# Optimization experiments

Measured on AMD Instinct MI355X. Metric: run time of the kernel, lower is better.

Reference implementation:

```python
import jax, jax.numpy as jnp
import numpy as np

HID = 256
NUM_ENT = 100000
NUM_REL = 50
E = 320000  # edges per direction; edge_index has 2*E columns
BN_EPS = 1e-5


def setup_inputs() -> dict:
    key = jax.random.key(0)
    ks = jax.random.split(key, 10)
    x = jax.random.normal(ks[0], (NUM_ENT, HID), dtype=jnp.float32)
    edge_index = jax.random.randint(ks[1], (2, 2 * E), 0, NUM_ENT)
    edge_type = jax.random.randint(ks[2], (2 * E,), 0, NUM_REL)
    rel_embed = jax.random.normal(ks[3], (NUM_REL, HID), dtype=jnp.float32)
    # xavier_normal init: std = sqrt(2 / (fan_in + fan_out))
    w_std = (2.0 / (HID + HID)) ** 0.5
    w_loop = jax.random.normal(ks[4], (HID, HID), dtype=jnp.float32) * w_std
    w_in = jax.random.normal(ks[5], (HID, HID), dtype=jnp.float32) * w_std
    w_out = jax.random.normal(ks[6], (HID, HID), dtype=jnp.float32) * w_std
    w_rel = jax.random.normal(ks[7], (HID, HID), dtype=jnp.float32) * w_std
    loop_rel = jax.random.normal(ks[8], (1, HID), dtype=jnp.float32) * ((2.0 / (1 + HID)) ** 0.5)
    bn_weight = jnp.ones((HID,), dtype=jnp.float32)
    bn_bias = jnp.zeros((HID,), dtype=jnp.float32)
    return {
        "x": x, "edge_index": edge_index, "edge_type": edge_type,
        "rel_embed": rel_embed, "w_loop": w_loop, "w_in": w_in,
        "w_out": w_out, "w_rel": w_rel, "loop_rel": loop_rel,
        "bn_weight": bn_weight, "bn_bias": bn_bias,
    }


def _compute_norm(edge_index, num_ent):
    # symmetric D^-1/2 * D^-1/2 norm; degree counted on row (target) index
    row, col = edge_index[0], edge_index[1]
    deg = jax.ops.segment_sum(jnp.ones_like(row, dtype=jnp.float32), row, num_segments=num_ent)
    deg_inv = jnp.where(deg > 0, deg ** -0.5, 0.0)
    return deg_inv[row] * deg_inv[col]


def _propagate(x, idx, etype, rel_all, W, norm, num_ent):
    # gather source nodes (idx[1]), compose with relation emb (mult), transform, scale, scatter-add to targets (idx[0])
    msg = (x[idx[1]] * rel_all[etype]) @ W  # [E, d]
    if norm is not None:
        msg = msg * norm[:, None]
    return jax.ops.segment_sum(msg, idx[0], num_segments=num_ent)


def reference(x, edge_index, edge_type, rel_embed, w_loop, w_in, w_out, w_rel,
              loop_rel, bn_weight, bn_bias):
    num_ent = x.shape[0]
    rel_all = jnp.concatenate([rel_embed, loop_rel], axis=0)  # [R+1, d]
    e = edge_index.shape[1] // 2
    in_index, out_index = edge_index[:, :e], edge_index[:, e:]
    in_type, out_type = edge_type[:e], edge_type[e:]

    in_norm = _compute_norm(in_index, num_ent)
    out_norm = _compute_norm(out_index, num_ent)

    in_res = _propagate(x, in_index, in_type, rel_all, w_in, in_norm, num_ent)
    out_res = _propagate(x, out_index, out_type, rel_all, w_out, out_norm, num_ent)
    # self-loop: identity scatter -> just per-node compose+transform
    loop_res = (x * loop_rel) @ w_loop

    out = (in_res + out_res + loop_res) * (1.0 / 3.0)

    # BatchNorm1d in training mode (batch stats, biased variance)
    mean = out.mean(axis=0)
    var = out.var(axis=0)
    out = (out - mean) * jax.lax.rsqrt(var + BN_EPS) * bn_weight + bn_bias

    rel_out = (rel_all @ w_rel)[:-1]  # drop loop relation
    return out, rel_out
```

## Files before the change

kernel.cpp:

```cpp
#include <hip/hip_runtime.h>

#define HID     256
#define N_ENT   100000
#define TOT_E   640000
#define HALF_E  320000
#define NSEG    (2 * N_ENT)
#define BN_EPSF 1e-5f
#define SCAN_ELEMS 1024
#define NBLK_SCAN  ((NSEG + SCAN_ELEMS - 1) / SCAN_ELEMS)

typedef short bf16x8 __attribute__((ext_vector_type(8)));
typedef short bf16x4 __attribute__((ext_vector_type(4)));
typedef float f32x4  __attribute__((ext_vector_type(4)));

__device__ __forceinline__ short f2b(float f) {
    union { float f; unsigned u; } c; c.f = f;
    unsigned u = c.u;
    u += 0x7FFF + ((u >> 16) & 1);
    return (short)(u >> 16);
}
__device__ __forceinline__ float b2f(short b) {
    union { unsigned u; float f; } c;
    c.u = ((unsigned)(unsigned short)b) << 16;
    return c.f;
}

#define NX8 (N_ENT * HID / 8)
#define NR8 (50 * HID / 8)
#define CONV_BLOCKS ((NX8 + NR8 + 255) / 256)
__global__ void prep_kernel(const float* __restrict__ x, short* __restrict__ xh,
                            const float* __restrict__ rel, short* __restrict__ relh,
                            const float* __restrict__ w_in, const float* __restrict__ w_out,
                            const float* __restrict__ w_loop, const float* __restrict__ loop_rel,
                            short* __restrict__ WT,
                            int* __restrict__ offs, float* __restrict__ stats) {
    int bid = blockIdx.x;
    int tid = threadIdx.x;
    if (bid < CONV_BLOCKS) {
        int i = bid * 256 + tid;
        if (i < NSEG) offs[i] = 0;
        if (i < 512) stats[i] = 0.f;
        const float* src; short* dst; int idx;
        if (i < NX8) { src = x; dst = xh; idx = i; }
        else if (i < NX8 + NR8) { src = rel; dst = relh; idx = i - NX8; }
        else return;
        const float4* p = (const float4*)(src + (size_t)idx * 8);
        float4 v0 = p[0], v1 = p[1];
        bf16x8 pk;
        pk[0]=f2b(v0.x); pk[1]=f2b(v0.y); pk[2]=f2b(v0.z); pk[3]=f2b(v0.w);
        pk[4]=f2b(v1.x); pk[5]=f2b(v1.y); pk[6]=f2b(v1.z); pk[7]=f2b(v1.w);
        *(bf16x8*)(dst + (size_t)idx * 8) = pk;
    } else {
        int n = bid - CONV_BLOCKS;
        int t = tid;
        float v0 = w_in  [(size_t)t * HID + n];
        float v1 = w_out [(size_t)t * HID + n];
        float v2 = w_loop[(size_t)t * HID + n] * loop_rel[t];
        short* row = WT + (size_t)n * 768;
        row[t]       = f2b(v0);
        row[256 + t] = f2b(v1);
        row[512 + t] = f2b(v2);
    }
}

__global__ void hist_kernel(const int* __restrict__ ei, int* __restrict__ offs) {
    int j = blockIdx.x * 256 + threadIdx.x;
    if (j >= TOT_E) return;
    int seg = ei[j] + ((j < HALF_E) ? 0 : N_ENT);
    atomicAdd(&offs[seg], 1);
}

__global__ __launch_bounds__(256) void scan1(int* __restrict__ offs, int* __restrict__ bsums,
                                             float* __restrict__ rnorm) {
    __shared__ int tsum[256];
    int b = blockIdx.x, t = threadIdx.x;
    int base = b * SCAN_ELEMS + t * 4;
    int v[4] = {0, 0, 0, 0};
    if (base + 3 < NSEG) {
        int4 lv = *(const int4*)(offs + base);
        v[0] = lv.x; v[1] = lv.y; v[2] = lv.z; v[3] = lv.w;
    } else {
        for (int i = 0; i < 4; ++i) if (base + i < NSEG) v[i] = offs[base + i];
    }
    #pragma unroll
    for (int i = 0; i < 4; ++i)
        if (base + i < NSEG)
            rnorm[base + i] = (v[i] > 0) ? rsqrtf((float)v[i]) : 0.f;
    tsum[t] = v[0] + v[1] + v[2] + v[3];
    __syncthreads();
    for (int d = 1; d < 256; d <<= 1) {
        int val = (t >= d) ? tsum[t - d] : 0;
        __syncthreads();
        tsum[t] += val;
        __syncthreads();
    }
    int run = (t == 0) ? 0 : tsum[t - 1];
    if (t == 255) bsums[b] = tsum[255];
    int w[4];
    for (int i = 0; i < 4; ++i) { w[i] = run; run += v[i]; }
    if (base + 3 < NSEG) *(int4*)(offs + base) = make_int4(w[0], w[1], w[2], w[3]);
    else for (int i = 0; i < 4; ++i) if (base + i < NSEG) offs[base + i] = w[i];
}

__global__ __launch_bounds__(256) void scan3f(int* __restrict__ offs, const int* __restrict__ bsums) {
    __shared__ int tmp[256];
    int b = blockIdx.x, t = threadIdx.x;
    tmp[t] = (t < NBLK_SCAN) ? bsums[t] : 0;
    __syncthreads();
    for (int d = 1; d < 256; d <<= 1) {
        int val = (t >= d) ? tmp[t - d] : 0;
        __syncthreads();
        tmp[t] += val;
        __syncthreads();
    }
    int add = (b == 0) ? 0 : tmp[b - 1];
    int base = b * SCAN_ELEMS + t * 4;
    if (base + 3 < NSEG) {
        int4 v = *(int4*)(offs + base);
        v.x += add; v.y += add; v.z += add; v.w += add;
        *(int4*)(offs + base) = v;
    } else {
        for (int i = 0; i < 4; ++i) if (base + i < NSEG) offs[base + i] += add;
    }
}

__global__ void fill8_kernel(const int* __restrict__ ei, const int* __restrict__ et,
                             int* __restrict__ offs, const float* __restrict__ rnorm,
                             int2* __restrict__ elist8) {
    int j = blockIdx.x * 256 + threadIdx.x;
    if (j >= TOT_E) return;
    int hb  = (j < HALF_E) ? 0 : N_ENT;
    int seg = ei[j] + hb;
    int col = ei[TOT_E + j];
    float norm = rnorm[seg] * rnorm[hb + col];
    int pos = atomicAdd(&offs[seg], 1);
    elist8[pos] = make_int2(col | (et[j] << 17), __float_as_int(norm));
}

__global__ __launch_bounds__(256) void gather_h(
        const short* __restrict__ xh, const short* __restrict__ relh,
        const int* __restrict__ offs, const int2* __restrict__ elist8,
        short* __restrict__ accA, short* __restrict__ accB) {
    int s = blockIdx.x * 4 + (threadIdx.x >> 6);
    int lane = threadIdx.x & 63;
    int start = (s == 0) ? 0 : offs[s - 1];
    int end   = offs[s];
    float ax0=0.f, ay0=0.f, az0=0.f, aw0=0.f;
    float ax1=0.f, ay1=0.f, az1=0.f, aw1=0.f;
    int e = start;
    for (; e + 2 <= end; e += 2) {
        int2 p0 = elist8[e];
        int2 p1 = elist8[e + 1];
        int   c0 = p0.x & 0x1FFFF, t0 = p0.x >> 17;
        float n0 = __int_as_float(p0.y);
        int   c1 = p1.x & 0x1FFFF, t1 = p1.x >> 17;
        float n1 = __int_as_float(p1.y);
        bf16x4 xv0 = *(const bf16x4*)(xh   + (size_t)c0 * HID + lane * 4);
        bf16x4 rv0 = *(const bf16x4*)(relh + (size_t)t0 * HID + lane * 4);
        bf16x4 xv1 = *(const bf16x4*)(xh   + (size_t)c1 * HID + lane * 4);
        bf16x4 rv1 = *(const bf16x4*)(relh + (size_t)t1 * HID + lane * 4);
        ax0 += b2f(xv0[0]) * b2f(rv0[0]) * n0;
        ay0 += b2f(xv0[1]) * b2f(rv0[1]) * n0;
        az0 += b2f(xv0[2]) * b2f(rv0[2]) * n0;
        aw0 += b2f(xv0[3]) * b2f(rv0[3]) * n0;
        ax1 += b2f(xv1[0]) * b2f(rv1[0]) * n1;
        ay1 += b2f(xv1[1]) * b2f(rv1[1]) * n1;
        az1 += b2f(xv1[2]) * b2f(rv1[2]) * n1;
        aw1 += b2f(xv1[3]) * b2f(rv1[3]) * n1;
    }
    if (e < end) {
        int2 p = elist8[e];
        int   c = p.x & 0x1FFFF, t = p.x >> 17;
        float n = __int_as_float(p.y);
        bf16x4 xv = *(const bf16x4*)(xh   + (size_t)c * HID + lane * 4);
        bf16x4 rv = *(const bf16x4*)(relh + (size_t)t * HID + lane * 4);
        ax0 += b2f(xv[0]) * b2f(rv[0]) * n;
        ay0 += b2f(xv[1]) * b2f(rv[1]) * n;
        az0 += b2f(xv[2]) * b2f(rv[2]) * n;
        aw0 += b2f(xv[3]) * b2f(rv[3]) * n;
    }
    int hb = (s >= N_ENT) ? N_ENT : 0;
    short* dst = ((s >= N_ENT) ? accB : accA) + (size_t)(s - hb) * HID + lane * 4;
    bf16x4 pk;
    pk[0] = f2b(ax0 + ax1); pk[1] = f2b(ay0 + ay1);
    pk[2] = f2b(az0 + az1); pk[3] = f2b(aw0 + aw1);
    *(bf16x4*)dst = pk;
}

template <bool BF16OUT>
__global__ __launch_bounds__(256) void gemm_mfma_h(
        const short* __restrict__ accA, const short* __restrict__ accB,
        const short* __restrict__ xh, const short* __restrict__ WT,
        float* __restrict__ out, short* __restrict__ outh, float* __restrict__ stats)
{
    __shared__ __align__(16) short As[64 * 64];
    __shared__ __align__(16) short Bs[256 * 64];
    const int tid = threadIdx.x;
    const int l   = tid & 63;
    const int wid = tid >> 6;
    const int r0  = blockIdx.x * 64;
    const int lr  = l & 15;
    const int lg  = l >> 4;

    f32x4 acc[4][4];
    #pragma unroll
    for (int i = 0; i < 4; ++i)
        #pragma unroll
        for (int j = 0; j < 4; ++j)
            acc[i][j] = (f32x4){0.f, 0.f, 0.f, 0.f};

    const int sg = tid & 7;
    const int sr = tid >> 3;

    for (int kt = 0; kt < 12; ++kt) {
        const int src = kt >> 2;
        const short* Ap = (src == 0) ? accA : ((src == 1) ? accB : xh);
        const int ksg = kt * 64;
        const int ksl = (kt & 3) * 64;
        __syncthreads();
        #pragma unroll
        for (int h = 0; h < 2; ++h) {
            int r  = sr + 32 * h;
            int gr = r0 + r;
            bf16x8 v = {0,0,0,0,0,0,0,0};
            if (gr < N_ENT) v = *(const bf16x8*)(Ap + (size_t)gr * HID + ksl + sg * 8);
            *(bf16x8*)&As[r * 64 + ((sg ^ (r & 7)) << 3)] = v;
        }
        #pragma unroll
        for (int i = 0; i < 8; ++i) {
            int n = sr + 32 * i;
            bf16x8 w = *(const bf16x8*)(WT + (size_t)n * 768 + ksg + sg * 8);
            *(bf16x8*)&Bs[n * 64 + ((sg ^ (n & 7)) << 3)] = w;
        }
        __syncthreads();
        #pragma unroll
        for (int kc = 0; kc < 2; ++kc) {
            const int gsel = kc * 4 + lg;
            bf16x8 af[4], bfr[4];
            #pragma unroll
            for (int i = 0; i < 4; ++i) {
                int r = 16 * i + lr;
                af[i] = *(const bf16x8*)&As[r * 64 + ((gsel ^ (r & 7)) << 3)];
            }
            #pragma unroll
            for (int j = 0; j < 4; ++j) {
                int n = wid * 64 + 16 * j + lr;
                bfr[j] = *(const bf16x8*)&Bs[n * 64 + ((gsel ^ (n & 7)) << 3)];
            }
            #pragma unroll
            for (int i = 0; i < 4; ++i)
                #pragma unroll
                for (int j = 0; j < 4; ++j)
                    acc[i][j] = __builtin_amdgcn_mfma_f32_16x16x32_bf16(
                                    af[i], bfr[j], acc[i][j], 0, 0, 0);
        }
    }

    const float third = 1.f / 3.f;
    float s[4]  = {0.f, 0.f, 0.f, 0.f};
    float sq[4] = {0.f, 0.f, 0.f, 0.f};
    #pragma unroll
    for (int i = 0; i < 4; ++i) {
        #pragma unroll
        for (int v = 0; v < 4; ++v) {
            int grow = r0 + 16 * i + lg * 4 + v;
            if (grow < N_ENT) {
                #pragma unroll
                for (int j = 0; j < 4; ++j) {
                    float val = acc[i][j][v] * third;
                    int col = wid * 64 + 16 * j + lr;
                    if (BF16OUT) outh[(size_t)grow * HID + col] = f2b(val);
                    else         out [(size_t)grow * HID + col] = val;
                    s[j] += val; sq[j] += val * val;
                }
            }
        }
    }
    #pragma unroll
    for (int j = 0; j < 4; ++j) {
        s[j]  += __shfl_xor(s[j], 16);  s[j]  += __shfl_xor(s[j], 32);
        sq[j] += __shfl_xor(sq[j], 16); sq[j] += __shfl_xor(sq[j], 32);
    }
    if (lg == 0) {
        #pragma unroll
        for (int j = 0; j < 4; ++j) {
            int c = wid * 64 + 16 * j + lr;
            atomicAdd(&stats[c], s[j]);
            atomicAdd(&stats[HID + c], sq[j]);
        }
    }
}

#define BN_BLOCKS 1024
__global__ void bn_relout_h(const short* __restrict__ outh, float* __restrict__ out,
                            const float* __restrict__ stats,
                            const float* __restrict__ bnw, const float* __restrict__ bnb,
                            const float* __restrict__ rel_embed, const float* __restrict__ w_rel,
                            float* __restrict__ rel_out) {
    if (blockIdx.x < BN_BLOCKS) {
        const float invN = 1.f / (float)N_ENT;
        const int total8 = N_ENT * (HID / 8);
        for (int i = blockIdx.x * 256 + threadIdx.x; i < total8; i += BN_BLOCKS * 256) {
            int c = (i & 31) * 8;
            bf16x8 v = *(const bf16x8*)(outh + (size_t)i * 8);
            float r[8];
            #pragma unroll
            for (int k = 0; k < 8; ++k) {
                float mean = stats[c + k] * invN;
                float var  = stats[HID + c + k] * invN - mean * mean;
                float sc   = rsqrtf(var + BN_EPSF) * bnw[c + k];
                float sh   = bnb[c + k] - mean * sc;
                r[k] = b2f(v[k]) * sc + sh;
            }
            float4* dst = (float4*)(out + (size_t)i * 8);
            dst[0] = make_float4(r[0], r[1], r[2], r[3]);
            dst[1] = make_float4(r[4], r[5], r[6], r[7]);
        }
    } else {
        __shared__ float row[HID];
        int r = blockIdx.x - BN_BLOCKS;
        int c = threadIdx.x;
        row[c] = rel_embed[(size_t)r * HID + c];
        __syncthreads();
        float sum = 0.f;
        #pragma unroll 8
        for (int k = 0; k < HID; ++k) sum += row[k] * w_rel[(size_t)k * HID + c];
        rel_out[(size_t)r * HID + c] = sum;
    }
}

__global__ void bn_relout_f(float* __restrict__ out, const float* __restrict__ stats,
                            const float* __restrict__ bnw, const float* __restrict__ bnb,
                            const float* __restrict__ rel_embed, const float* __restrict__ w_rel,
                            float* __restrict__ rel_out) {
    if (blockIdx.x < BN_BLOCKS) {
        const float invN = 1.f / (float)N_ENT;
        const int total4 = N_ENT * (HID / 4);
        for (int i = blockIdx.x * 256 + threadIdx.x; i < total4; i += BN_BLOCKS * 256) {
            int c = (i & 63) * 4;
            float4 v = *(float4*)(out + (size_t)i * 4);
            #pragma unroll
            for (int k = 0; k < 4; ++k) {
                float mean = stats[c + k] * invN;
                float var  = stats[HID + c + k] * invN - mean * mean;
                float sc   = rsqrtf(var + BN_EPSF) * bnw[c + k];
                float sh   = bnb[c + k] - mean * sc;
                float* comp = (k == 0) ? &v.x : (k == 1) ? &v.y : (k == 2) ? &v.z : &v.w;
                *comp = (*comp) * sc + sh;
            }
            *(float4*)(out + (size_t)i * 4) = v;
        }
    } else {
        __shared__ float row[HID];
        int r = blockIdx.x - BN_BLOCKS;
        int c = threadIdx.x;
        row[c] = rel_embed[(size_t)r * HID + c];
        __syncthreads();
        float sum = 0.f;
        #pragma unroll 8
        for (int k = 0; k < HID; ++k) sum += row[k] * w_rel[(size_t)k * HID + c];
        rel_out[(size_t)r * HID + c] = sum;
    }
}

extern "C" void kernel_launch(void* const* d_in, const int* in_sizes, int n_in,
                              void* d_out, int out_size, void* d_ws, size_t ws_size,
                              hipStream_t stream) {
    const float* x        = (const float*)d_in[0];
    const int*   ei       = (const int*)d_in[1];
    const int*   et       = (const int*)d_in[2];
    const float* rel      = (const float*)d_in[3];
    const float* w_loop   = (const float*)d_in[4];
    const float* w_in     = (const float*)d_in[5];
    const float* w_out    = (const float*)d_in[6];
    const float* w_rel    = (const float*)d_in[7];
    const float* loop_rel = (const float*)d_in[8];
    const float* bnw      = (const float*)d_in[9];
    const float* bnb      = (const float*)d_in[10];

    float* out     = (float*)d_out;
    float* rel_out = out + (size_t)N_ENT * HID;

    const size_t XH_B   = (size_t)N_ENT * HID * 2;
    const size_t ACC_B  = (size_t)N_ENT * HID * 2;
    const size_t OFFS_B = (size_t)NSEG * 4;
    const size_t EL8_B  = (size_t)TOT_E * 8;
    const size_t RN_B   = (size_t)NSEG * 4;
    const size_t RELH_B = (size_t)50 * HID * 2;
    const size_t WT_B   = (size_t)256 * 768 * 2;
    const size_t base_need = XH_B + 2 * ACC_B + OFFS_B + EL8_B + RN_B
                           + 256 * 4 + 512 * 4 + RELH_B + WT_B;
    const size_t OUTH_B = (size_t)N_ENT * HID * 2;
    const bool   have_outh = (ws_size >= base_need + OUTH_B);

    char* w = (char*)d_ws;
    short* xh     = (short*)w;              w += XH_B;
    short* accA_h = (short*)w;              w += ACC_B;
    short* accB_h = (short*)w;              w += ACC_B;
    int*   offs   = (int*)w;                w += OFFS_B;
    int2*  elist8 = (int2*)w;               w += EL8_B;
    float* rnorm  = (float*)w;              w += RN_B;
    int*   bsums  = (int*)w;                w += 256 * 4;
    float* stats  = (float*)w;              w += 512 * 4;
    short* relh   = (short*)w;              w += RELH_B;
    short* WT     = (short*)w;              w += WT_B;
    short* outh   = (short*)w;

    prep_kernel<<<CONV_BLOCKS + 256, 256, 0, stream>>>(x, xh, rel, relh,
                                                       w_in, w_out, w_loop, loop_rel,
                                                       WT, offs, stats);
    hist_kernel<<<TOT_E / 256, 256, 0, stream>>>(ei, offs);
    scan1<<<NBLK_SCAN, 256, 0, stream>>>(offs, bsums, rnorm);
    scan3f<<<NBLK_SCAN, 256, 0, stream>>>(offs, bsums);
    fill8_kernel<<<TOT_E / 256, 256, 0, stream>>>(ei, et, offs, rnorm, elist8);
    gather_h<<<NSEG / 4, 256, 0, stream>>>(xh, relh, offs, elist8, accA_h, accB_h);
    if (have_outh) {
        gemm_mfma_h<true><<<(N_ENT + 63) / 64, 256, 0, stream>>>(
            accA_h, accB_h, xh, WT, out, outh, stats);
        bn_relout_h<<<BN_BLOCKS + 50, 256, 0, stream>>>(outh, out, stats, bnw, bnb,
                                                        rel, w_rel, rel_out);
    } else {
        gemm_mfma_h<false><<<(N_ENT + 63) / 64, 256, 0, stream>>>(
            accA_h, accB_h, xh, WT, out, outh, stats);
        bn_relout_f<<<BN_BLOCKS + 50, 256, 0, stream>>>(out, stats, bnw, bnb,
                                                        rel, w_rel, rel_out);
    }
}
```

Before: 308.4 us.

## Triple-buffer GEMM tiles with direct global-to-LDS async loads

```diff
diff --git a/kernel.cpp b/kernel.cpp
--- a/kernel.cpp
+++ b/kernel.cpp
@@ -23,6 +23,11 @@
     union { unsigned u; float f; } c;
     c.u = ((unsigned)(unsigned short)b) << 16;
     return c.f;
+}
+__device__ __forceinline__ void gload16(const void* g, void* l) {
+    __builtin_amdgcn_global_load_lds(
+        (const __attribute__((address_space(1))) unsigned*)(g),
+        (__attribute__((address_space(3))) unsigned*)(l), 16, 0, 0);
 }
 
 #define NX8 (N_ENT * HID / 8)
@@ -188,13 +193,13 @@
 }
 
 template <bool BF16OUT>
-__global__ __launch_bounds__(256) void gemm_mfma_h(
+__global__ __launch_bounds__(256) void gemm_pipe(
         const short* __restrict__ accA, const short* __restrict__ accB,
         const short* __restrict__ xh, const short* __restrict__ WT,
         float* __restrict__ out, short* __restrict__ outh, float* __restrict__ stats)
 {
-    __shared__ __align__(16) short As[64 * 64];
-    __shared__ __align__(16) short Bs[256 * 64];
+    __shared__ __align__(16) short As[3][64 * 64];
+    __shared__ __align__(16) short Bs[3][256 * 64];
     const int tid = threadIdx.x;
     const int l   = tid & 63;
     const int wid = tid >> 6;
@@ -209,30 +214,38 @@
         for (int j = 0; j < 4; ++j)
             acc[i][j] = (f32x4){0.f, 0.f, 0.f, 0.f};
 
-    const int sg = tid & 7;
-    const int sr = tid >> 3;
-
-    for (int kt = 0; kt < 12; ++kt) {
+    auto stage = [&](int buf, int kt) {
         const int src = kt >> 2;
         const short* Ap = (src == 0) ? accA : ((src == 1) ? accB : xh);
+        const int ksl = (kt & 3) * 64;
         const int ksg = kt * 64;
-        const int ksl = (kt & 3) * 64;
-        __syncthreads();
         #pragma unroll
         for (int h = 0; h < 2; ++h) {
-            int r  = sr + 32 * h;
+            int c  = wid * 2 + h;
+            int r  = c * 8 + (l >> 3);
+            int sg = (l & 7) ^ (r & 7);
             int gr = r0 + r;
-            bf16x8 v = {0,0,0,0,0,0,0,0};
-            if (gr < N_ENT) v = *(const bf16x8*)(Ap + (size_t)gr * HID + ksl + sg * 8);
-            *(bf16x8*)&As[r * 64 + ((sg ^ (r & 7)) << 3)] = v;
+            if (gr >= N_ENT) gr = N_ENT - 1;
+            gload16(Ap + (size_t)gr * HID + ksl + sg * 8, &As[buf][c * 512]);
         }
         #pragma unroll
         for (int i = 0; i < 8; ++i) {
-            int n = sr + 32 * i;
-            bf16x8 w = *(const bf16x8*)(WT + (size_t)n * 768 + ksg + sg * 8);
-            *(bf16x8*)&Bs[n * 64 + ((sg ^ (n & 7)) << 3)] = w;
-        }
-        __syncthreads();
+            int c  = wid * 8 + i;
+            int n  = c * 8 + (l >> 3);
+            int sg = (l & 7) ^ (n & 7);
+            gload16(WT + (size_t)n * 768 + ksg + sg * 8, &Bs[buf][c * 512]);
+        }
+    };
+
+    stage(0, 0);
+    stage(1, 1);
+    for (int kt = 0; kt < 12; ++kt) {
+        if (kt < 11) { asm volatile("s_waitcnt vmcnt(10)" ::: "memory"); }
+        else         { asm volatile("s_waitcnt vmcnt(0)"  ::: "memory"); }
+        __builtin_amdgcn_s_barrier();
+        __builtin_amdgcn_sched_barrier(0);
+        if (kt + 2 < 12) stage((kt + 2) % 3, kt + 2);
+        const int cur = kt % 3;
         #pragma unroll
         for (int kc = 0; kc < 2; ++kc) {
             const int gsel = kc * 4 + lg;
@@ -240,12 +253,12 @@
             #pragma unroll
             for (int i = 0; i < 4; ++i) {
                 int r = 16 * i + lr;
-                af[i] = *(const bf16x8*)&As[r * 64 + ((gsel ^ (r & 7)) << 3)];
+                af[i] = *(const bf16x8*)&As[cur][r * 64 + ((gsel ^ (r & 7)) << 3)];
             }
             #pragma unroll
             for (int j = 0; j < 4; ++j) {
                 int n = wid * 64 + 16 * j + lr;
-                bfr[j] = *(const bf16x8*)&Bs[n * 64 + ((gsel ^ (n & 7)) << 3)];
+                bfr[j] = *(const bf16x8*)&Bs[cur][n * 64 + ((gsel ^ (n & 7)) << 3)];
             }
             #pragma unroll
             for (int i = 0; i < 4; ++i)
@@ -415,12 +428,12 @@
     fill8_kernel<<<TOT_E / 256, 256, 0, stream>>>(ei, et, offs, rnorm, elist8);
     gather_h<<<NSEG / 4, 256, 0, stream>>>(xh, relh, offs, elist8, accA_h, accB_h);
     if (have_outh) {
-        gemm_mfma_h<true><<<(N_ENT + 63) / 64, 256, 0, stream>>>(
+        gemm_pipe<true><<<(N_ENT + 63) / 64, 256, 0, stream>>>(
             accA_h, accB_h, xh, WT, out, outh, stats);
         bn_relout_h<<<BN_BLOCKS + 50, 256, 0, stream>>>(outh, out, stats, bnw, bnb,
                                                         rel, w_rel, rel_out);
     } else {
-        gemm_mfma_h<false><<<(N_ENT + 63) / 64, 256, 0, stream>>>(
+        gemm_pipe<false><<<(N_ENT + 63) / 64, 256, 0, stream>>>(
             accA_h, accB_h, xh, WT, out, outh, stats);
         bn_relout_f<<<BN_BLOCKS + 50, 256, 0, stream>>>(out, stats, bnw, bnb,
                                                         rel, w_rel, rel_out);
```

After: 361.1 us. 1.17x slower.
